# Performance work log

Measured on AMD Instinct MI355X. Metric: run time of the kernel, lower is better.

Reference implementation:

```python
import jax, jax.numpy as jnp
import numpy as np

B, C, H, W = 4, 32, 32, 1024
PATCH = 21           # patch_size in spatial_correlation_sample
DIL = 2              # dilation_patch
PAD = DIL * (PATCH - 1) // 2  # 20: max displacement, zero-padded out-of-range samples


def setup_inputs() -> dict:
    key = jax.random.key(0)
    k1, k2 = jax.random.split(key)
    x1 = jax.random.normal(k1, (B, C, H, W), dtype=jnp.float32)
    x2 = jax.random.normal(k2, (B, C, H, W), dtype=jnp.float32)
    return {"x1": x1, "x2": x2}


def _correlate(x1, x2):
    # spatial_correlation_sample(kernel_size=1, patch_size=21, stride=1,
    #                            padding=0, dilation_patch=2)
    # out[b, pi, pj, h, w] = sum_c x1[b,c,h,w] * x2[b,c,h+2*(pi-10), w+2*(pj-10)]
    # with out-of-bounds x2 samples treated as zero.
    b, c, h, w = x1.shape
    x2p = jnp.pad(x2, ((0, 0), (0, 0), (PAD, PAD), (PAD, PAD)))
    chans = []
    for i in range(PATCH):      # fixed 21x21 displacement grid (static slices)
        for j in range(PATCH):
            win = jax.lax.slice(x2p, (0, 0, DIL * i, DIL * j),
                                (b, c, DIL * i + h, DIL * j + w))
            chans.append(jnp.einsum('bchw,bchw->bhw', x1, win))
    corr = jnp.stack(chans, axis=1) / c  # (b, 441, h, w), normalized by n_channels
    return jax.nn.leaky_relu(corr, negative_slope=0.1)


def reference(x1, x2):
    # CorrelationNetwork.forward returns only out_correlation; the conv/deconv
    # flow pyramid does not contribute to the returned tensor (and the
    # visualize_flow calls reference undefined symbols in the original).
    return _correlate(x1, x2)
```

## Files before the change

### kernel.cpp

```cpp
#include <hip/hip_runtime.h>

#define BB    4
#define CC    32
#define HH    32
#define WW    1024
#define PATCH 21
#define DIL   2
#define RAD   10
#define PADW  20
#define CHUNK 4
#define LROW  (WW + 2*PADW)

template <int PJ0, int TPT>
__device__ __forceinline__ void corr_body(const float* __restrict__ x1,
                                          const float* __restrict__ x2,
                                          float* __restrict__ out,
                                          float* __restrict__ sx2 ) {
    const int tid = threadIdx.x;
    const int h   = blockIdx.x;
    const int bp  = blockIdx.y;
    const int b   = bp / PATCH;
    const int pi  = bp - b * PATCH;
    const int r2  = h + DIL * (pi - RAD);
    const int w4  = tid * 4;

    float* outp = out + (((size_t)(b * PATCH * PATCH + pi * PATCH + PJ0)) * HH + h) * WW + w4;

    if (r2 < 0 || r2 >= HH) {
        float4 z = make_float4(0.f, 0.f, 0.f, 0.f);
#pragma unroll
        for (int j = 0; j < TPT; j++)
            *(float4*)(outp + (size_t)j * HH * WW) = z;
        return;
    }

    const float* x1p = x1 + (((size_t)(b * CC) * HH + h) * WW) + w4;
    const float* x2p = x2 + (((size_t)(b * CC) * HH + r2) * WW);

    float acc[TPT][4];
#pragma unroll
    for (int j = 0; j < TPT; j++)
#pragma unroll
        for (int k = 0; k < 4; k++) acc[j][k] = 0.f;

    for (int cc = 0; cc < CC; cc += CHUNK) {
        __syncthreads();
        for (int idx = tid; idx < CHUNK * (LROW / 4); idx += 256) {
            int c  = idx / (LROW / 4);
            int i4 = idx - c * (LROW / 4);
            int u  = i4 * 4 - PADW;
            float4 v = make_float4(0.f, 0.f, 0.f, 0.f);
            if (u >= 0 && u <= WW - 4)
                v = *(const float4*)(x2p + (size_t)(cc + c) * HH * WW + u);
            *(float4*)&sx2[c * LROW + i4 * 4] = v;
        }
        __syncthreads();

#pragma unroll
        for (int c = 0; c < CHUNK; c++) {
            float4 av = *(const float4*)(x1p + (size_t)(cc + c) * HH * WW);
            const float a[4] = {av.x, av.y, av.z, av.w};

            constexpr int WFL = 4 + 2 * (TPT - 1);
            constexpr int WV  = (WFL + 3) / 4;
            float win[WV * 4];
            const float* wbase = &sx2[c * LROW + w4 + 2 * PJ0];
#pragma unroll
            for (int v = 0; v < WV; v++)
                *(float4*)&win[v * 4] = *(const float4*)(wbase + v * 4);

#pragma unroll
            for (int j = 0; j < TPT; j++)
#pragma unroll
                for (int k = 0; k < 4; k++)
                    acc[j][k] = fmaf(a[k], win[2 * j + k], acc[j][k]);
        }
    }

    const float inv_c = 1.0f / (float)CC;
#pragma unroll
    for (int j = 0; j < TPT; j++) {
        float4 o;
        float* ov = (float*)&o;
#pragma unroll
        for (int k = 0; k < 4; k++) {
            float v = acc[j][k] * inv_c;
            ov[k] = v > 0.f ? v : 0.1f * v;
        }
        *(float4*)(outp + (size_t)j * HH * WW) = o;
    }
}

__global__ __launch_bounds__(256, 8)
void corr_kernel(const float* __restrict__ x1, const float* __restrict__ x2,
                 float* __restrict__ out) {
    __shared__ float sx2[CHUNK * LROW];
    if (blockIdx.z == 0)      corr_body<0, 8>(x1, x2, out, sx2);
    else if (blockIdx.z == 1) corr_body<8, 8>(x1, x2, out, sx2);
    else                      corr_body<16, 5>(x1, x2, out, sx2);
}

extern "C" void kernel_launch(void* const* d_in, const int* in_sizes, int n_in,
                              void* d_out, int out_size, void* d_ws, size_t ws_size,
                              hipStream_t stream) {
    const float* x1 = (const float*)d_in[0];
    const float* x2 = (const float*)d_in[1];
    float* out = (float*)d_out;

    dim3 grid(HH, BB * PATCH, 3);
    dim3 block(256, 1, 1);
    corr_kernel<<<grid, block, 0, stream>>>(x1, x2, out);
}
```

Measured before the change: 327.5 us.

## Compute all 21 horizontal displacements per block with a rolling register window

```diff
diff --git a/kernel.cpp b/kernel.cpp
--- a/kernel.cpp
+++ b/kernel.cpp
@@ -11,11 +11,11 @@
 #define CHUNK 4
 #define LROW  (WW + 2*PADW)
 
-template <int PJ0, int TPT>
-__device__ __forceinline__ void corr_body(const float* __restrict__ x1,
-                                          const float* __restrict__ x2,
-                                          float* __restrict__ out,
-                                          float* __restrict__ sx2 ) {
+__global__ __launch_bounds__(256, 4)
+void corr_kernel(const float* __restrict__ x1, const float* __restrict__ x2,
+                 float* __restrict__ out) {
+    __shared__ float sx2[CHUNK * LROW];
+
     const int tid = threadIdx.x;
     const int h   = blockIdx.x;
     const int bp  = blockIdx.y;
@@ -24,12 +24,12 @@
     const int r2  = h + DIL * (pi - RAD);
     const int w4  = tid * 4;
 
-    float* outp = out + (((size_t)(b * PATCH * PATCH + pi * PATCH + PJ0)) * HH + h) * WW + w4;
+    float* outp = out + (((size_t)(b * PATCH * PATCH + pi * PATCH)) * HH + h) * WW + w4;
 
     if (r2 < 0 || r2 >= HH) {
         float4 z = make_float4(0.f, 0.f, 0.f, 0.f);
 #pragma unroll
-        for (int j = 0; j < TPT; j++)
+        for (int j = 0; j < PATCH; j++)
             *(float4*)(outp + (size_t)j * HH * WW) = z;
         return;
     }
@@ -37,9 +37,9 @@
     const float* x1p = x1 + (((size_t)(b * CC) * HH + h) * WW) + w4;
     const float* x2p = x2 + (((size_t)(b * CC) * HH + r2) * WW);
 
-    float acc[TPT][4];
+    float acc[PATCH][4];
 #pragma unroll
-    for (int j = 0; j < TPT; j++)
+    for (int j = 0; j < PATCH; j++)
 #pragma unroll
         for (int k = 0; k < 4; k++) acc[j][k] = 0.f;
 
@@ -61,25 +61,25 @@
             float4 av = *(const float4*)(x1p + (size_t)(cc + c) * HH * WW);
             const float a[4] = {av.x, av.y, av.z, av.w};
 
-            constexpr int WFL = 4 + 2 * (TPT - 1);
-            constexpr int WV  = (WFL + 3) / 4;
-            float win[WV * 4];
-            const float* wbase = &sx2[c * LROW + w4 + 2 * PJ0];
+            const float* wb = &sx2[c * LROW + w4];
+            float ring[12];
+            *(float4*)&ring[0] = *(const float4*)(wb);
 #pragma unroll
-            for (int v = 0; v < WV; v++)
-                *(float4*)&win[v * 4] = *(const float4*)(wbase + v * 4);
-
-#pragma unroll
-            for (int j = 0; j < TPT; j++)
+            for (int j = 0; j < PATCH; j++) {
+                if (j & 1) {
+                    const int f = (j + 1) >> 1;
+                    *(float4*)&ring[(f % 3) * 4] = *(const float4*)(wb + 4 * f);
+                }
 #pragma unroll
                 for (int k = 0; k < 4; k++)
-                    acc[j][k] = fmaf(a[k], win[2 * j + k], acc[j][k]);
+                    acc[j][k] = fmaf(a[k], ring[(2 * j + k) % 12], acc[j][k]);
+            }
         }
     }
 
     const float inv_c = 1.0f / (float)CC;
 #pragma unroll
-    for (int j = 0; j < TPT; j++) {
+    for (int j = 0; j < PATCH; j++) {
         float4 o;
         float* ov = (float*)&o;
 #pragma unroll
@@ -91,15 +91,6 @@
     }
 }
 
-__global__ __launch_bounds__(256, 8)
-void corr_kernel(const float* __restrict__ x1, const float* __restrict__ x2,
-                 float* __restrict__ out) {
-    __shared__ float sx2[CHUNK * LROW];
-    if (blockIdx.z == 0)      corr_body<0, 8>(x1, x2, out, sx2);
-    else if (blockIdx.z == 1) corr_body<8, 8>(x1, x2, out, sx2);
-    else                      corr_body<16, 5>(x1, x2, out, sx2);
-}
-
 extern "C" void kernel_launch(void* const* d_in, const int* in_sizes, int n_in,
                               void* d_out, int out_size, void* d_ws, size_t ws_size,
                               hipStream_t stream) {
@@ -107,7 +98,7 @@
     const float* x2 = (const float*)d_in[1];
     float* out = (float*)d_out;
 
-    dim3 grid(HH, BB * PATCH, 3);
+    dim3 grid(HH, BB * PATCH, 1);
     dim3 block(256, 1, 1);
     corr_kernel<<<grid, block, 0, stream>>>(x1, x2, out);
 }
```

Result: slower. 369.3 us (+12.8%).
